# Kernel tuning notes

Measured on AMD Instinct MI355X. Metric: run time of the kernel, lower is better.

## Reference

```python
import jax, jax.numpy as jnp
import numpy as np

COST_CLASS, COST_BBOX, COST_GIOU = 1.0, 5.0, 2.0


def _cxcywh_to_xyxy(b):
    cx, cy, w, h = b[..., 0], b[..., 1], b[..., 2], b[..., 3]
    return jnp.stack([cx - 0.5 * w, cy - 0.5 * h, cx + 0.5 * w, cy + 0.5 * h], axis=-1)


def _generalized_box_iou(boxes1, boxes2):
    # boxes1 [N,4], boxes2 [M,4] in xyxy -> [N,M] GIoU
    area1 = (boxes1[:, 2] - boxes1[:, 0]) * (boxes1[:, 3] - boxes1[:, 1])
    area2 = (boxes2[:, 2] - boxes2[:, 0]) * (boxes2[:, 3] - boxes2[:, 1])
    lt = jnp.maximum(boxes1[:, None, :2], boxes2[None, :, :2])
    rb = jnp.minimum(boxes1[:, None, 2:], boxes2[None, :, 2:])
    wh = jnp.clip(rb - lt, 0.0)
    inter = wh[..., 0] * wh[..., 1]
    union = area1[:, None] + area2[None, :] - inter
    iou = inter / union
    lt_e = jnp.minimum(boxes1[:, None, :2], boxes2[None, :, :2])
    rb_e = jnp.maximum(boxes1[:, None, 2:], boxes2[None, :, 2:])
    wh_e = jnp.clip(rb_e - lt_e, 0.0)
    area_e = wh_e[..., 0] * wh_e[..., 1]
    return iou - (area_e - union) / area_e


def setup_inputs() -> dict:
    key = jax.random.key(0)
    k1, k2, k3, k4 = jax.random.split(key, 4)
    B, Q, NC, T = 16, 900, 92, 1600
    return {
        "class_logits": jax.random.normal(k1, (B, Q, NC), dtype=jnp.float32),
        "box_regression": jax.random.uniform(k2, (B, Q, 4), dtype=jnp.float32),
        "tgt_ids": jax.random.randint(k3, (T,), 0, NC, dtype=jnp.int64),
        "tgt_bbox": jax.random.uniform(k4, (T, 4), dtype=jnp.float32),
    }


def reference(class_logits, box_regression, tgt_ids, tgt_bbox):
    B, Q, NC = class_logits.shape
    out_prob = jax.nn.softmax(class_logits.reshape(B * Q, NC), axis=-1)  # [BQ, NC]
    out_bbox = box_regression.reshape(B * Q, 4)                          # [BQ, 4]
    cost_class = -out_prob[:, tgt_ids]                                   # [BQ, T]
    cost_bbox = jnp.sum(jnp.abs(out_bbox[:, None, :] - tgt_bbox[None, :, :]), axis=-1)  # L1 cdist
    cost_giou = -_generalized_box_iou(_cxcywh_to_xyxy(out_bbox), _cxcywh_to_xyxy(tgt_bbox))
    C = COST_BBOX * cost_bbox + COST_CLASS * cost_class + COST_GIOU * cost_giou
    return C.reshape(B, Q, -1)
```

## Files before the change

### kernel.cpp

```cpp
#include <hip/hip_runtime.h>
#include <math.h>

#define BB 16
#define QQ 900
#define NC 92
#define NCP 96
#define TT 1600
#define BQ (BB * QQ)

#define RT 2
#define RTILE 8
#define NK 25

__global__ __launch_bounds__(256)
void k_cost(const float* __restrict__ logits,
            const float* __restrict__ boxes,
            const int* __restrict__ tids,
            const float* __restrict__ tbox,
            float* __restrict__ out) {
    __shared__ float pexp[RTILE][NCP];

    const int row0 = blockIdx.x * RTILE;

    {
        int idx = threadIdx.x * 2;
        int r = idx / NCP, c = idx - r * NCP;
        float2 v = make_float2(0.0f, 0.0f);
        if (c < NC) {
            float2 lv = *(const float2*)&logits[(row0 + r) * NC + c];
            v.x = __expf(lv.x); v.y = __expf(lv.y);
        }
        *(float2*)&pexp[r][c] = v;
        if (threadIdx.x < 128) {
            int idx2 = 512 + threadIdx.x * 2;
            int r2 = idx2 / NCP, c2 = idx2 - r2 * NCP;
            float2 v2 = make_float2(0.0f, 0.0f);
            if (c2 < NC) {
                float2 lv = *(const float2*)&logits[(row0 + r2) * NC + c2];
                v2.x = __expf(lv.x); v2.y = __expf(lv.y);
            }
            *(float2*)&pexp[r2][c2] = v2;
        }
    }

    const int tl   = threadIdx.x & 63;
    const int rg   = threadIdx.x >> 6;
    const int rloc = rg * RT;
    const int rbase = row0 + rloc;

    float rcx[RT], rcy[RT], rw[RT], rh[RT];
    float rx0[RT], ry0[RT], rx1[RT], ry1[RT], rar[RT];
    #pragma unroll
    for (int j = 0; j < RT; ++j) {
        float4 bb = ((const float4*)boxes)[rbase + j];
        rcx[j] = bb.x; rcy[j] = bb.y; rw[j] = bb.z; rh[j] = bb.w;
        rx0[j] = bb.x - 0.5f * bb.z; ry0[j] = bb.y - 0.5f * bb.w;
        rx1[j] = bb.x + 0.5f * bb.z; ry1[j] = bb.y + 0.5f * bb.w;
        rar[j] = bb.z * bb.w;
    }
    __syncthreads();

    float rinv[RT];
    {
        const int lr = tl >> 5;
        const int ls = tl & 31;
        float s = pexp[rloc + lr][ls * 3]
                + pexp[rloc + lr][ls * 3 + 1]
                + pexp[rloc + lr][ls * 3 + 2];
        s += __shfl_xor(s, 1);
        s += __shfl_xor(s, 2);
        s += __shfl_xor(s, 4);
        s += __shfl_xor(s, 8);
        s += __shfl_xor(s, 16);
        rinv[0] = __builtin_amdgcn_rcpf(__shfl(s, 0));
        rinv[1] = __builtin_amdgcn_rcpf(__shfl(s, 32));
    }

    float* o0 = out + rbase * TT + tl;
    #pragma unroll 5
    for (int k = 0; k < NK; ++k) {
        const int t = k * 64 + tl;
        float4 tb = ((const float4*)tbox)[t];
        int    id = tids[t];
        float tx0 = tb.x - 0.5f * tb.z, ty0 = tb.y - 0.5f * tb.w;
        float tx1 = tb.x + 0.5f * tb.z, ty1 = tb.y + 0.5f * tb.w;
        float tar = tb.z * tb.w;
        #pragma unroll
        for (int j = 0; j < RT; ++j) {
            float l1 = fabsf(rcx[j] - tb.x) + fabsf(rcy[j] - tb.y)
                     + fabsf(rw[j]  - tb.z) + fabsf(rh[j]  - tb.w);
            float iwu = fminf(rx1[j], tx1) - fmaxf(rx0[j], tx0);
            float ihu = fminf(ry1[j], ty1) - fmaxf(ry0[j], ty0);
            float inter = fmaxf(iwu, 0.0f) * fmaxf(ihu, 0.0f);
            float uni = rar[j] + tar - inter;
            float ew = (rw[j] + tb.z) - iwu;
            float eh = (rh[j] + tb.w) - ihu;
            float ea = ew * eh;
            float num = fmaf(ea, inter - uni, uni * uni);
            float rden = __builtin_amdgcn_rcpf(uni * ea);
            float p = pexp[rloc + j][id];
            float c = fmaf(-p, rinv[j], 5.0f * l1);
            c = fmaf(-2.0f * num, rden, c);
            __builtin_nontemporal_store(c, o0 + j * TT + k * 64);
        }
    }
}

extern "C" void kernel_launch(void* const* d_in, const int* in_sizes, int n_in,
                              void* d_out, int out_size, void* d_ws, size_t ws_size,
                              hipStream_t stream) {
    const float* logits = (const float*)d_in[0];
    const float* boxes  = (const float*)d_in[1];
    const int*   tids   = (const int*)  d_in[2];
    const float* tbox   = (const float*)d_in[3];
    float* out = (float*)d_out;

    k_cost<<<dim3(BQ / RTILE, 1), 256, 0, stream>>>(
        logits, boxes, tids, tbox, out);
}
```

Before: 30.29 us.

## Pre-normalize softmax in shared memory, prefetch targets, use regular stores

Adds an extra barrier and a pass where 8 warps each normalize one row of the exponentiated logits in shared memory, so the inner loop no longer multiplies by a per-row reciprocal. The target box and id for the next iteration are software-prefetched into registers to hide global load latency. Output stores change from nontemporal to ordinary stores. This costs an extra __syncthreads, a shared-memory read-modify-write pass, and more live registers; the normal stores may pollute cache for the large output.

```diff
diff --git a/kernel.cpp b/kernel.cpp
--- a/kernel.cpp
+++ b/kernel.cpp
@@ -42,6 +42,25 @@
             *(float2*)&pexp[r2][c2] = v2;
         }
     }
+    __syncthreads();
+
+    {
+        const int r  = threadIdx.x >> 5;
+        const int ls = threadIdx.x & 31;
+        float a = pexp[r][ls * 3];
+        float b = pexp[r][ls * 3 + 1];
+        float d = pexp[r][ls * 3 + 2];
+        float s = a + b + d;
+        s += __shfl_xor(s, 1);
+        s += __shfl_xor(s, 2);
+        s += __shfl_xor(s, 4);
+        s += __shfl_xor(s, 8);
+        s += __shfl_xor(s, 16);
+        float rinv = __builtin_amdgcn_rcpf(s);
+        pexp[r][ls * 3]     = a * rinv;
+        pexp[r][ls * 3 + 1] = b * rinv;
+        pexp[r][ls * 3 + 2] = d * rinv;
+    }
 
     const int tl   = threadIdx.x & 63;
     const int rg   = threadIdx.x >> 6;
@@ -60,28 +79,16 @@
     }
     __syncthreads();
 
-    float rinv[RT];
-    {
-        const int lr = tl >> 5;
-        const int ls = tl & 31;
-        float s = pexp[rloc + lr][ls * 3]
-                + pexp[rloc + lr][ls * 3 + 1]
-                + pexp[rloc + lr][ls * 3 + 2];
-        s += __shfl_xor(s, 1);
-        s += __shfl_xor(s, 2);
-        s += __shfl_xor(s, 4);
-        s += __shfl_xor(s, 8);
-        s += __shfl_xor(s, 16);
-        rinv[0] = __builtin_amdgcn_rcpf(__shfl(s, 0));
-        rinv[1] = __builtin_amdgcn_rcpf(__shfl(s, 32));
-    }
-
     float* o0 = out + rbase * TT + tl;
+    float4 tb = ((const float4*)tbox)[tl];
+    int    id = tids[tl];
     #pragma unroll 5
     for (int k = 0; k < NK; ++k) {
-        const int t = k * 64 + tl;
-        float4 tb = ((const float4*)tbox)[t];
-        int    id = tids[t];
+        float4 tbn; int idn;
+        if (k + 1 < NK) {
+            tbn = ((const float4*)tbox)[(k + 1) * 64 + tl];
+            idn = tids[(k + 1) * 64 + tl];
+        }
         float tx0 = tb.x - 0.5f * tb.z, ty0 = tb.y - 0.5f * tb.w;
         float tx1 = tb.x + 0.5f * tb.z, ty1 = tb.y + 0.5f * tb.w;
         float tar = tb.z * tb.w;
@@ -99,10 +106,11 @@
             float num = fmaf(ea, inter - uni, uni * uni);
             float rden = __builtin_amdgcn_rcpf(uni * ea);
             float p = pexp[rloc + j][id];
-            float c = fmaf(-p, rinv[j], 5.0f * l1);
+            float c = fmaf(5.0f, l1, -p);
             c = fmaf(-2.0f * num, rden, c);
-            __builtin_nontemporal_store(c, o0 + j * TT + k * 64);
+            o0[j * TT + k * 64] = c;
         }
+        tb = tbn; id = idn;
     }
 }
 
```

Result: faster. 28.14 us (-7.1%).
